# Kernel optimization log

Hardware: AMD Instinct MI355X
Metric: run time of the kernel (lower is better)

Reference implementation:

```python
import jax, jax.numpy as jnp
import numpy as np

B = 32768
NUM_CLASS = 1000
FEATURE_DIM = 512


def setup_inputs() -> dict:
    key = jax.random.key(0)
    k1, k2, k3 = jax.random.split(key, 3)
    features = jax.random.normal(k1, (B, FEATURE_DIM), dtype=jnp.float32)
    labels = jax.random.randint(k2, (B,), 0, NUM_CLASS, dtype=jnp.int32)
    center = jax.random.normal(k3, (NUM_CLASS, FEATURE_DIM), dtype=jnp.float32)
    return {"features": features, "labels": labels, "center": center}


def reference(features, labels, center):
    C = center.shape[0]
    # ---- intra loss: per-row euclidean distance to own-class center ----
    # (equivalent to gathering dist_mat[i, labels[i]] from cdist(features, center, p=2))
    diff = features - center[labels]                      # [B, D]
    dist = jnp.sqrt(jnp.sum(diff * diff, axis=-1))        # [B]
    dist = jnp.clip(dist, 1e-12, 1e12)
    intra_loss = dist.mean()

    # ---- inter loss ----
    # torch: center.scatter_add(0, labels_rep, features) -> center_param + per-class sum
    sums = jax.ops.segment_sum(features, labels, num_segments=C)          # [C, D]
    # counts: scatter_add with index [B,1] only uses first column of ones -> class counts
    counts = jax.ops.segment_sum(jnp.ones((features.shape[0],), features.dtype),
                                 labels, num_segments=C)                  # [C]
    cen = (center + sums) / jnp.clip(counts, 1.0, None)[:, None]          # [C, D]
    # source bug: loop keeps only the LAST combination (C-2, C-1)
    d_last = jnp.sqrt(jnp.sum((cen[C - 2] - cen[C - 1]) ** 2))
    inter_loss = (2.0 / d_last) * (1.0 / (C * (C - 1)))
    return (intra_loss, inter_loss)
```

## Files before the change

### kernel.cpp

```cpp
#include <hip/hip_runtime.h>

#define B_ROWS   32768
#define NUM_CLS  1000
#define FEAT     512

#define INTER_BLOCKS    16
#define INTRA_BLOCKS    4096
#define THREADS         256
#define WAVES_PER_BLOCK 4
#define ROWS_PER_WAVE   2
#define TOTAL_WAVES     (INTRA_BLOCKS * WAVES_PER_BLOCK)
#define LABELS_PER_IB   (B_ROWS / INTER_BLOCKS)
#define LISTCAP         128

typedef float f32x4 __attribute__((ext_vector_type(4)));
typedef float f32x2 __attribute__((ext_vector_type(2)));

#define WS_INTER 16384
#define SLOT     1032

__global__ __launch_bounds__(THREADS, 8) void loss_pass1(
    const float* __restrict__ features,
    const int*   __restrict__ labels,
    const float* __restrict__ center,
    float*       __restrict__ ws)
{
    if (blockIdx.x < INTER_BLOCKS) {
        const int ib = blockIdx.x;
        const int t  = threadIdx.x;

        __shared__ int list[LISTCAP];
        __shared__ int nm_s;
        if (t == 0) nm_s = 0;
        __syncthreads();

        const int4* lab4 = (const int4*)(labels + ib * LABELS_PER_IB);
        #pragma unroll
        for (int k = 0; k < 2; ++k) {
            const int j = t + k * 256;
            int4 L = lab4[j];
            const int row0 = ib * LABELS_PER_IB + 4 * j;
            if (L.x >= NUM_CLS - 2) { int i = atomicAdd(&nm_s, 1); if (i < LISTCAP) list[i] = (row0 << 1)       | (L.x - (NUM_CLS - 2)); }
            if (L.y >= NUM_CLS - 2) { int i = atomicAdd(&nm_s, 1); if (i < LISTCAP) list[i] = ((row0 + 1) << 1) | (L.y - (NUM_CLS - 2)); }
            if (L.z >= NUM_CLS - 2) { int i = atomicAdd(&nm_s, 1); if (i < LISTCAP) list[i] = ((row0 + 2) << 1) | (L.z - (NUM_CLS - 2)); }
            if (L.w >= NUM_CLS - 2) { int i = atomicAdd(&nm_s, 1); if (i < LISTCAP) list[i] = ((row0 + 3) << 1) | (L.w - (NUM_CLS - 2)); }
        }
        __syncthreads();
        const int nm = min(nm_s, LISTCAP);

        float s0a = 0.0f, s0b = 0.0f, s1a = 0.0f, s1b = 0.0f;
        int c0 = 0, c1 = 0;
        for (int m = 0; m < nm; ++m) {
            const int e   = list[m];
            const int row = e >> 1;
            const f32x2 v = ((const f32x2*)(features + (size_t)row * FEAT))[t];
            if (e & 1) { s1a += v.x; s1b += v.y; ++c1; }
            else       { s0a += v.x; s0b += v.y; ++c0; }
        }

        float* slot = ws + WS_INTER + ib * SLOT;
        if (t == 0) { slot[0] = (float)c0; slot[1] = (float)c1; }
        f32x2 v0; v0.x = s0a; v0.y = s0b;
        f32x2 v1; v1.x = s1a; v1.y = s1b;
        ((f32x2*)(slot + 2))[t]   = v0;
        ((f32x2*)(slot + 514))[t] = v1;
        return;
    }

    const int bid  = blockIdx.x - INTER_BLOCKS;
    const int lane = threadIdx.x & 63;
    const int wave = __builtin_amdgcn_readfirstlane(threadIdx.x >> 6);
    const int wid  = bid * WAVES_PER_BLOCK + wave;
    const int base_row = wid * ROWS_PER_WAVE;

    const int lab0 = labels[base_row];
    const int lab1 = labels[base_row + 1];

    const f32x4* f0p = (const f32x4*)(features + (size_t)base_row * FEAT);
    const f32x4* f1p = (const f32x4*)(features + (size_t)(base_row + 1) * FEAT);
    const f32x4* c0p = (const f32x4*)(center   + (size_t)lab0 * FEAT);
    const f32x4* c1p = (const f32x4*)(center   + (size_t)lab1 * FEAT);

    f32x4 fa = f0p[lane];
    f32x4 fb = f0p[lane + 64];
    f32x4 fc = f1p[lane];
    f32x4 fd = f1p[lane + 64];
    f32x4 ca = c0p[lane];
    f32x4 cb = c0p[lane + 64];
    f32x4 cc = c1p[lane];
    f32x4 cd = c1p[lane + 64];

    f32x4 d0 = fa - ca, d1 = fb - cb, d2 = fc - cc, d3 = fd - cd;
    float p0 = d0.x*d0.x + d0.y*d0.y + d0.z*d0.z + d0.w*d0.w
             + d1.x*d1.x + d1.y*d1.y + d1.z*d1.z + d1.w*d1.w;
    float p1 = d2.x*d2.x + d2.y*d2.y + d2.z*d2.z + d2.w*d2.w
             + d3.x*d3.x + d3.y*d3.y + d3.z*d3.z + d3.w*d3.w;

    const bool b0 = lane & 1;
    float send = b0 ? p0 : p1;
    float keep = b0 ? p1 : p0;
    float u = keep + __shfl_xor(send, 1);
    u += __shfl_xor(u, 2);
    u += __shfl_xor(u, 4);
    u += __shfl_xor(u, 8);
    u += __shfl_xor(u, 16);
    u += __shfl_xor(u, 32);
    float dist = sqrtf(u);
    dist = fminf(fmaxf(dist, 1e-12f), 1e12f);
    dist += __shfl_xor(dist, 1);

    if (lane == 0)
        ws[wid] = dist;
}

__global__ __launch_bounds__(512) void loss_pass2(
    const float* __restrict__ center,
    const float* __restrict__ ws,
    float*       __restrict__ out)
{
    const int t = threadIdx.x;

    float cnt0 = 0.0f, cnt1 = 0.0f;
    #pragma unroll
    for (int b = 0; b < INTER_BLOCKS; ++b) {
        const float* slot = ws + WS_INTER + b * SLOT;
        cnt0 += slot[0];
        cnt1 += slot[1];
    }
    cnt0 = fmaxf(cnt0, 1.0f);
    cnt1 = fmaxf(cnt1, 1.0f);

    float s0 = 0.0f, s1 = 0.0f;
    #pragma unroll
    for (int b = 0; b < INTER_BLOCKS; ++b) {
        const float* slot = ws + WS_INTER + b * SLOT;
        s0 += slot[2 + t];
        s1 += slot[514 + t];
    }

    float a  = (center[(size_t)(NUM_CLS - 2) * FEAT + t] + s0) / cnt0;
    float bb = (center[(size_t)(NUM_CLS - 1) * FEAT + t] + s1) / cnt1;
    float df = a - bb;
    float p_inter = df * df;

    const f32x4* part4 = (const f32x4*)ws;
    float p_intra = 0.0f;
    #pragma unroll
    for (int k = 0; k < 8; ++k) {
        f32x4 v = part4[t + k * 512];
        p_intra += (v.x + v.y) + (v.z + v.w);
    }

    #pragma unroll
    for (int off = 32; off; off >>= 1) {
        p_inter += __shfl_xor(p_inter, off);
        p_intra += __shfl_xor(p_intra, off);
    }

    __shared__ float si[8], sa[8];
    if ((t & 63) == 0) { si[t >> 6] = p_inter; sa[t >> 6] = p_intra; }
    __syncthreads();

    if (t == 0) {
        float s_inter = 0.0f, s_intra = 0.0f;
        #pragma unroll
        for (int i = 0; i < 8; ++i) { s_inter += si[i]; s_intra += sa[i]; }
        float d_last = sqrtf(s_inter);
        out[0] = s_intra * (1.0f / (float)B_ROWS);
        out[1] = (2.0f / d_last) * (1.0f / ((float)NUM_CLS * (float)(NUM_CLS - 1)));
    }
}

extern "C" void kernel_launch(void* const* d_in, const int* in_sizes, int n_in,
                              void* d_out, int out_size, void* d_ws, size_t ws_size,
                              hipStream_t stream) {
    const float* features = (const float*)d_in[0];
    const int*   labels   = (const int*)d_in[1];
    const float* center   = (const float*)d_in[2];
    float* out = (float*)d_out;
    float* ws  = (float*)d_ws;

    loss_pass1<<<INTER_BLOCKS + INTRA_BLOCKS, THREADS, 0, stream>>>(features, labels, center, ws);
    loss_pass2<<<1, 512, 0, stream>>>(center, ws, out);
}
```

Measured before the change: 21.44 us.

## Process eight rows per wave with double-buffered loads in intra pass

Each wave now handles eight rows instead of two, with four times fewer intra blocks, and loads the next pair of rows while reducing the current pair. The partial-sum workspace shrinks, so the second pass reads fewer partials. The aim is to keep more memory requests in flight per wave and cut block launch and reduction overhead. In exchange, register pressure rises (the launch bound drops to four blocks per SM) and fewer waves are resident.

```diff
diff --git a/kernel.cpp b/kernel.cpp
--- a/kernel.cpp
+++ b/kernel.cpp
@@ -5,10 +5,10 @@
 #define FEAT     512
 
 #define INTER_BLOCKS    16
-#define INTRA_BLOCKS    4096
+#define INTRA_BLOCKS    1024
 #define THREADS         256
 #define WAVES_PER_BLOCK 4
-#define ROWS_PER_WAVE   2
+#define ROWS_PER_WAVE   8
 #define TOTAL_WAVES     (INTRA_BLOCKS * WAVES_PER_BLOCK)
 #define LABELS_PER_IB   (B_ROWS / INTER_BLOCKS)
 #define LISTCAP         128
@@ -16,10 +16,43 @@
 typedef float f32x4 __attribute__((ext_vector_type(4)));
 typedef float f32x2 __attribute__((ext_vector_type(2)));
 
-#define WS_INTER 16384
+#define WS_INTER 4096
 #define SLOT     1032
 
-__global__ __launch_bounds__(THREADS, 8) void loss_pass1(
+#define LOADPAIR(ROW, FA,FB,FC,FD, CA,CB,CC,CD) do {                         \
+    const int _lab0 = labels[(ROW)];                                         \
+    const int _lab1 = labels[(ROW) + 1];                                     \
+    const f32x4* _f0 = (const f32x4*)(features + (size_t)(ROW) * FEAT);      \
+    const f32x4* _f1 = (const f32x4*)(features + (size_t)((ROW)+1) * FEAT);  \
+    const f32x4* _c0 = (const f32x4*)(center + (size_t)_lab0 * FEAT);        \
+    const f32x4* _c1 = (const f32x4*)(center + (size_t)_lab1 * FEAT);        \
+    FA = _f0[lane]; FB = _f0[lane + 64];                                     \
+    FC = _f1[lane]; FD = _f1[lane + 64];                                     \
+    CA = _c0[lane]; CB = _c0[lane + 64];                                     \
+    CC = _c1[lane]; CD = _c1[lane + 64];                                     \
+} while (0)
+
+#define REDUCE2(FA,FB,FC,FD, CA,CB,CC,CD) ({                                 \
+    f32x4 _d0 = FA - CA, _d1 = FB - CB, _d2 = FC - CC, _d3 = FD - CD;        \
+    float _p0 = _d0.x*_d0.x + _d0.y*_d0.y + _d0.z*_d0.z + _d0.w*_d0.w        \
+              + _d1.x*_d1.x + _d1.y*_d1.y + _d1.z*_d1.z + _d1.w*_d1.w;       \
+    float _p1 = _d2.x*_d2.x + _d2.y*_d2.y + _d2.z*_d2.z + _d2.w*_d2.w        \
+              + _d3.x*_d3.x + _d3.y*_d3.y + _d3.z*_d3.z + _d3.w*_d3.w;       \
+    const bool _b0 = lane & 1;                                               \
+    float _send = _b0 ? _p0 : _p1;                                           \
+    float _keep = _b0 ? _p1 : _p0;                                           \
+    float _u = _keep + __shfl_xor(_send, 1);                                 \
+    _u += __shfl_xor(_u, 2);                                                 \
+    _u += __shfl_xor(_u, 4);                                                 \
+    _u += __shfl_xor(_u, 8);                                                 \
+    _u += __shfl_xor(_u, 16);                                                \
+    _u += __shfl_xor(_u, 32);                                                \
+    float _dist = sqrtf(_u);                                                 \
+    _dist = fminf(fmaxf(_dist, 1e-12f), 1e12f);                              \
+    _dist + __shfl_xor(_dist, 1);                                            \
+})
+
+__global__ __launch_bounds__(THREADS, 4) void loss_pass1(
     const float* __restrict__ features,
     const int*   __restrict__ labels,
     const float* __restrict__ center,
@@ -73,44 +106,22 @@
     const int wid  = bid * WAVES_PER_BLOCK + wave;
     const int base_row = wid * ROWS_PER_WAVE;
 
-    const int lab0 = labels[base_row];
-    const int lab1 = labels[base_row + 1];
+    f32x4 fa0, fb0, fc0, fd0, ca0, cb0, cc0, cd0;
+    f32x4 fa1, fb1, fc1, fd1, ca1, cb1, cc1, cd1;
 
-    const f32x4* f0p = (const f32x4*)(features + (size_t)base_row * FEAT);
-    const f32x4* f1p = (const f32x4*)(features + (size_t)(base_row + 1) * FEAT);
-    const f32x4* c0p = (const f32x4*)(center   + (size_t)lab0 * FEAT);
-    const f32x4* c1p = (const f32x4*)(center   + (size_t)lab1 * FEAT);
+    float acc;
 
-    f32x4 fa = f0p[lane];
-    f32x4 fb = f0p[lane + 64];
-    f32x4 fc = f1p[lane];
-    f32x4 fd = f1p[lane + 64];
-    f32x4 ca = c0p[lane];
-    f32x4 cb = c0p[lane + 64];
-    f32x4 cc = c1p[lane];
-    f32x4 cd = c1p[lane + 64];
-
-    f32x4 d0 = fa - ca, d1 = fb - cb, d2 = fc - cc, d3 = fd - cd;
-    float p0 = d0.x*d0.x + d0.y*d0.y + d0.z*d0.z + d0.w*d0.w
-             + d1.x*d1.x + d1.y*d1.y + d1.z*d1.z + d1.w*d1.w;
-    float p1 = d2.x*d2.x + d2.y*d2.y + d2.z*d2.z + d2.w*d2.w
-             + d3.x*d3.x + d3.y*d3.y + d3.z*d3.z + d3.w*d3.w;
-
-    const bool b0 = lane & 1;
-    float send = b0 ? p0 : p1;
-    float keep = b0 ? p1 : p0;
-    float u = keep + __shfl_xor(send, 1);
-    u += __shfl_xor(u, 2);
-    u += __shfl_xor(u, 4);
-    u += __shfl_xor(u, 8);
-    u += __shfl_xor(u, 16);
-    u += __shfl_xor(u, 32);
-    float dist = sqrtf(u);
-    dist = fminf(fmaxf(dist, 1e-12f), 1e12f);
-    dist += __shfl_xor(dist, 1);
+    LOADPAIR(base_row,     fa0, fb0, fc0, fd0, ca0, cb0, cc0, cd0);
+    LOADPAIR(base_row + 2, fa1, fb1, fc1, fd1, ca1, cb1, cc1, cd1);
+    acc  = REDUCE2(fa0, fb0, fc0, fd0, ca0, cb0, cc0, cd0);
+    LOADPAIR(base_row + 4, fa0, fb0, fc0, fd0, ca0, cb0, cc0, cd0);
+    acc += REDUCE2(fa1, fb1, fc1, fd1, ca1, cb1, cc1, cd1);
+    LOADPAIR(base_row + 6, fa1, fb1, fc1, fd1, ca1, cb1, cc1, cd1);
+    acc += REDUCE2(fa0, fb0, fc0, fd0, ca0, cb0, cc0, cd0);
+    acc += REDUCE2(fa1, fb1, fc1, fd1, ca1, cb1, cc1, cd1);
 
     if (lane == 0)
-        ws[wid] = dist;
+        ws[wid] = acc;
 }
 
 __global__ __launch_bounds__(512) void loss_pass2(
@@ -146,7 +157,7 @@
     const f32x4* part4 = (const f32x4*)ws;
     float p_intra = 0.0f;
     #pragma unroll
-    for (int k = 0; k < 8; ++k) {
+    for (int k = 0; k < 2; ++k) {
         f32x4 v = part4[t + k * 512];
         p_intra += (v.x + v.y) + (v.z + v.w);
     }
```

Result: no change. 21.67 us (+1.1%).
